# Kernel optimization log

Hardware: AMD Instinct MI355X
Metric: run time of the kernel (lower is better)

Reference implementation:

```python
import jax, jax.numpy as jnp
import numpy as np

BITS = 4
N_PACK = 32 // BITS  # 8
GROUPSIZE = 128
IN_FEATURES = 4096
OUT_FEATURES = 4096


def setup_inputs() -> dict:
    key = jax.random.key(0)
    k1, k2, k3, k4 = jax.random.split(key, 4)
    x = jax.random.normal(k1, (4, 2048, IN_FEATURES), dtype=jnp.float32)
    packed_weight = jax.random.randint(
        k2, (OUT_FEATURES, IN_FEATURES // N_PACK),
        jnp.iinfo(jnp.int32).min, jnp.iinfo(jnp.int32).max, dtype=jnp.int32)
    scale = jax.random.uniform(k3, (OUT_FEATURES, IN_FEATURES // GROUPSIZE),
                               dtype=jnp.float32, minval=0.001, maxval=0.02)
    bias = jax.random.normal(k4, (OUT_FEATURES,), dtype=jnp.float32) * 0.01
    return {"x": x, "packed_weight": packed_weight, "scale": scale, "bias": bias}


def _dequant_weight(packed_weight, scale):
    # Unpack 8 signed int4 values per int32 word (symmetric path, no zero-point).
    # Matches torch recover(): (w << (32 - bits*(n_pack - e))) >> (32 - bits)
    # with arithmetic right shift giving sign extension into int8 range [-8, 7].
    e = jnp.arange(N_PACK, dtype=jnp.int32)
    left = (32 - BITS * (N_PACK - e)).astype(jnp.int32)          # [n_pack]
    w = jnp.right_shift(
        jnp.left_shift(packed_weight[:, :, None], left[None, None, :]),
        32 - BITS)                                               # [O, P, n_pack]
    w = w.reshape(OUT_FEATURES, IN_FEATURES).astype(jnp.float32)
    # Per-group scale: in_features divisible by groupsize (no-remainder branch).
    w = (w.reshape(-1, GROUPSIZE) * scale.reshape(-1, 1)).reshape(OUT_FEATURES, IN_FEATURES)
    return w


def reference(x, packed_weight, scale, bias):
    w = _dequant_weight(packed_weight, scale)      # [O, I] fp32
    # F.linear: x @ w.T + bias
    return jnp.einsum('bsi,oi->bso', x, w) + bias
```

## Files before the change

### kernel.cpp

```cpp
#include <hip/hip_runtime.h>

typedef __bf16 bf16x4 __attribute__((ext_vector_type(4)));
typedef __bf16 bf16x8 __attribute__((ext_vector_type(8)));
typedef float  f32x4  __attribute__((ext_vector_type(4)));

#define M_DIM 8192
#define N_DIM 4096
#define K_DIM 4096

#define GLDS16(gptr, lptr)                                                     \
  __builtin_amdgcn_global_load_lds(                                            \
      (const __attribute__((address_space(1))) void*)(gptr),                   \
      (__attribute__((address_space(3))) void*)(lptr), 16, 0, 0)


__global__ __launch_bounds__(256) void dequant_w_kernel(
    const int* __restrict__ pw, const float* __restrict__ scale,
    unsigned short* __restrict__ wbf) {
  int idx = blockIdx.x * 256 + threadIdx.x;
  int o = idx >> 9;
  int p = idx & 511;
  int w = pw[idx];
  float s = scale[o * 32 + (p >> 4)];
  bf16x8 v;
#pragma unroll
  for (int e = 0; e < 8; ++e) {
    int val = (int)((unsigned)w << (4 * e)) >> 28;
    v[e] = (__bf16)((float)val * s);
  }
  *(bf16x8*)&wbf[(size_t)idx * 8] = v;
}

__global__ __launch_bounds__(256) void conv_x_kernel(
    const float* __restrict__ x, unsigned short* __restrict__ xbf) {
  size_t i = (size_t)(blockIdx.x * 256 + threadIdx.x) * 4;
  float4 a = *(const float4*)&x[i];
  bf16x4 v = {(__bf16)a.x, (__bf16)a.y, (__bf16)a.z, (__bf16)a.w};
  *(bf16x4*)&xbf[i] = v;
}


template <int QM, int QN>
__device__ __forceinline__ void mfma_quad(f32x4 (&acc)[8][4],
                                          const bf16x8 (&a)[4][2],
                                          const bf16x8 (&b)[2][2]) {
  __builtin_amdgcn_s_setprio(1);
#pragma unroll
  for (int mi = 0; mi < 4; ++mi)
#pragma unroll
    for (int ni = 0; ni < 2; ++ni)
#pragma unroll
      for (int kk = 0; kk < 2; ++kk)
        acc[QM * 4 + mi][QN * 2 + ni] =
            __builtin_amdgcn_mfma_f32_16x16x32_bf16(
                a[mi][kk], b[ni][kk], acc[QM * 4 + mi][QN * 2 + ni], 0, 0, 0);
  __builtin_amdgcn_s_setprio(0);
}

#define STAGE_A(qm_, tau_)                                                     \
  do {                                                                         \
    const int k0_ = ((tau_) & 63) * 64;                                        \
    char* const base_ = lds + ((tau_) & 1) * 32768;                            \
    const int c0_ = wave * 2, c1_ = wave * 2 + 1;                              \
    const int R0_ = (qm_) * 64 + (c0_ & 7) * 8 + (c0_ >> 3) * 128;             \
    const int R1_ = (qm_) * 64 + (c1_ & 7) * 8 + (c1_ >> 3) * 128;             \
    GLDS16(xbf + (size_t)(m0 + R0_ + rs8) * K_DIM + k0_ + cs8e,                \
           base_ + R0_ * 128);                                                 \
    GLDS16(xbf + (size_t)(m0 + R1_ + rs8) * K_DIM + k0_ + cs8e,                \
           base_ + R1_ * 128);                                                 \
  } while (0)

#define STAGE_B(qn_, tau_)                                                     \
  do {                                                                         \
    const int k0_ = ((tau_) & 63) * 64;                                        \
    char* const base_ = lds + 65536 + ((tau_) & 1) * 32768;                    \
    const int c0_ = wave * 2, c1_ = wave * 2 + 1;                              \
    const int R0_ = (qn_) * 32 + (c0_ >> 2) * 64 + (c0_ & 3) * 8;              \
    const int R1_ = (qn_) * 32 + (c1_ >> 2) * 64 + (c1_ & 3) * 8;              \
    GLDS16(wbf + (size_t)(n0 + R0_ + rs8) * K_DIM + k0_ + cs8e,                \
           base_ + R0_ * 128);                                                 \
    GLDS16(wbf + (size_t)(n0 + R1_ + rs8) * K_DIM + k0_ + cs8e,                \
           base_ + R1_ * 128);                                                 \
  } while (0)

#define READ_A(d_, qm_)                                                        \
  do {                                                                         \
    const char* pA_ = lds + (d_) * 32768 + (qm_) * 8192 + aRowOff;             \
    a[0][0] = *(const bf16x8*)(pA_ + 0 + b0);                                  \
    a[0][1] = *(const bf16x8*)(pA_ + 0 + b1);                                  \
    a[1][0] = *(const bf16x8*)(pA_ + 2048 + b0);                               \
    a[1][1] = *(const bf16x8*)(pA_ + 2048 + b1);                               \
    a[2][0] = *(const bf16x8*)(pA_ + 4096 + b0);                               \
    a[2][1] = *(const bf16x8*)(pA_ + 4096 + b1);                               \
    a[3][0] = *(const bf16x8*)(pA_ + 6144 + b0);                               \
    a[3][1] = *(const bf16x8*)(pA_ + 6144 + b1);                               \
  } while (0)

#define READ_B(d_, qn_, dst_)                                                  \
  do {                                                                         \
    const char* pB_ = lds + 65536 + (d_) * 32768 + (qn_) * 4096 + bRowOff;     \
    dst_[0][0] = *(const bf16x8*)(pB_ + 0 + b0);                               \
    dst_[0][1] = *(const bf16x8*)(pB_ + 0 + b1);                               \
    dst_[1][0] = *(const bf16x8*)(pB_ + 2048 + b0);                            \
    dst_[1][1] = *(const bf16x8*)(pB_ + 2048 + b1);                            \
  } while (0)

#define PH_MID                                                                 \
  do {                                                                         \
    asm volatile("" ::: "memory");                                             \
    __builtin_amdgcn_s_barrier();                                              \
  } while (0)

#define PH_END                                                                 \
  do {                                                                         \
    asm volatile("" ::: "memory");                                             \
    __builtin_amdgcn_s_barrier();                                              \
  } while (0)

#define VMW6 asm volatile("s_waitcnt vmcnt(6)" ::: "memory")

__global__ __launch_bounds__(512, 2) void gemm8_kernel(
    const unsigned short* __restrict__ xbf,
    const unsigned short* __restrict__ wbf,
    const float* __restrict__ bias, float* __restrict__ out) {
  __shared__ char lds[131072];

  int bid = blockIdx.x;
  int cpx = gridDim.x >> 3;
  int swz = (bid & 7) * cpx + (bid >> 3);
  int bm = swz >> 4;
  int bn = swz & 15;
  int m0 = bm * 256, n0 = bn * 256;

  int tid = threadIdx.x;
  int lane = tid & 63;
  int wave = tid >> 6;
  int wm = wave >> 2, wn = wave & 3;
  int lr = lane & 15, lk = lane >> 4, l7 = lane & 7;

  const int rs8 = lane >> 3;
  const int cs8e = ((lane & 7) ^ rs8) * 8;
  const int b0 = ((lk ^ l7) << 4);
  const int b1 = b0 ^ 64;
  const int aRowOff = (wm * 128 + lr) * 128;
  const int bRowOff = (wn * 64 + lr) * 128;

  f32x4 acc[8][4];
#pragma unroll
  for (int i = 0; i < 8; ++i)
#pragma unroll
    for (int jx = 0; jx < 4; ++jx) acc[i][jx] = (f32x4)0.0f;

  bf16x8 a[4][2], bq0[2][2], bq1[2][2];

  STAGE_A(0, 0);
  STAGE_B(1, 0);
  STAGE_A(1, 0);
  STAGE_B(0, 0);
  STAGE_A(0, 1);
  STAGE_B(1, 1);
  STAGE_A(1, 1);
  VMW6;
  asm volatile("" ::: "memory");
  __builtin_amdgcn_s_barrier();

  for (int j = 0; j < K_DIM / 128; ++j) {
    int t = 2 * j;
    READ_B(0, 0, bq0);
    READ_A(0, 0);
    STAGE_B(0, t + 1);
    PH_MID;
    mfma_quad<0, 0>(acc, a, bq0);
    PH_END;
    READ_B(0, 1, bq1);
    STAGE_A(0, t + 2);
    PH_MID;
    mfma_quad<0, 1>(acc, a, bq1);
    PH_END;
    READ_A(0, 1);
    STAGE_B(1, t + 2);
    PH_MID;
    mfma_quad<1, 1>(acc, a, bq1);
    PH_END;
    STAGE_A(1, t + 2);
    VMW6;
    PH_MID;
    mfma_quad<1, 0>(acc, a, bq0);
    PH_END;
    READ_B(1, 0, bq0);
    READ_A(1, 0);
    STAGE_B(0, t + 2);
    PH_MID;
    mfma_quad<0, 0>(acc, a, bq0);
    PH_END;
    READ_B(1, 1, bq1);
    STAGE_A(0, t + 3);
    PH_MID;
    mfma_quad<0, 1>(acc, a, bq1);
    PH_END;
    READ_A(1, 1);
    STAGE_B(1, t + 3);
    PH_MID;
    mfma_quad<1, 1>(acc, a, bq1);
    PH_END;
    STAGE_A(1, t + 3);
    VMW6;
    PH_MID;
    mfma_quad<1, 0>(acc, a, bq0);
    PH_END;
  }

  asm volatile("s_waitcnt vmcnt(0)" ::: "memory");

#pragma unroll
  for (int ng = 0; ng < 4; ++ng) {
    int col = n0 + wn * 64 + ng * 16 + lr;
    float bv = bias[col];
#pragma unroll
    for (int mg = 0; mg < 8; ++mg) {
      size_t rowb = (size_t)m0 + wm * 128 + mg * 16 + lk * 4;
#pragma unroll
      for (int r = 0; r < 4; ++r)
        out[(rowb + r) * N_DIM + col] = acc[mg][ng][r] + bv;
    }
  }
}

__global__ __launch_bounds__(256) void gemm_fused_kernel(
    const float* __restrict__ x, const int* __restrict__ pw,
    const float* __restrict__ scale, const float* __restrict__ bias,
    float* __restrict__ out) {
  __shared__ unsigned short As[128 * 64];
  __shared__ unsigned short Bs[128 * 64];
  int bid = blockIdx.x;
  int cpx = gridDim.x >> 3;
  int swz = (bid & 7) * cpx + (bid >> 3);
  int bm = swz >> 5, bn = swz & 31;
  int m0 = bm * 128, n0 = bn * 128;
  int tid = threadIdx.x;
  int lane = tid & 63;
  int wave = tid >> 6;
  int wm = wave >> 1, wn = wave & 1;
  int lr = lane & 15, lk = lane >> 4;
  f32x4 acc[4][4];
#pragma unroll
  for (int i = 0; i < 4; ++i)
#pragma unroll
    for (int jx = 0; jx < 4; ++jx) acc[i][jx] = (f32x4)0.0f;
  int tr = tid >> 4, tc = tid & 15;
  float4 ra[8];
  int4 rb;
  float sB = 0.f;
#pragma unroll
  for (int i = 0; i < 8; ++i)
    ra[i] = *(const float4*)&x[(size_t)(m0 + i * 16 + tr) * K_DIM + tc * 4];
  rb = *(const int4*)&pw[(size_t)(n0 + (tid >> 1)) * 512 + (tid & 1) * 4];
  sB = scale[(size_t)(n0 + (tid >> 1)) * 32 + 0];
  const int NT = K_DIM / 64;
  for (int t = 0; t < NT; ++t) {
#pragma unroll
    for (int i = 0; i < 8; ++i) {
      float4 v = ra[i];
      bf16x4 b4 = {(__bf16)v.x, (__bf16)v.y, (__bf16)v.z, (__bf16)v.w};
      *(bf16x4*)&As[(i * 16 + tr) * 64 + tc * 4] = b4;
    }
    {
      int n = tid >> 1, h = tid & 1;
#pragma unroll
      for (int w = 0; w < 4; ++w) {
        int word = ((const int*)&rb)[w];
        bf16x8 o;
#pragma unroll
        for (int e = 0; e < 8; ++e) {
          int val = (int)((unsigned)word << (4 * e)) >> 28;
          o[e] = (__bf16)((float)val * sB);
        }
        *(bf16x8*)&Bs[n * 64 + h * 32 + w * 8] = o;
      }
    }
    if (t + 1 < NT) {
      int k1 = (t + 1) * 64;
#pragma unroll
      for (int i = 0; i < 8; ++i)
        ra[i] = *(const float4*)&x[(size_t)(m0 + i * 16 + tr) * K_DIM + k1 +
                                   tc * 4];
      rb = *(const int4*)&pw[(size_t)(n0 + (tid >> 1)) * 512 + (k1 >> 3) +
                             (tid & 1) * 4];
      sB = scale[(size_t)(n0 + (tid >> 1)) * 32 + (k1 >> 7)];
    }
    __syncthreads();
#pragma unroll
    for (int kk = 0; kk < 2; ++kk) {
      bf16x8 af[4], bfr[4];
#pragma unroll
      for (int mi = 0; mi < 4; ++mi)
        af[mi] = *(const bf16x8*)&As[(wm * 64 + mi * 16 + lr) * 64 + kk * 32 +
                                     lk * 8];
#pragma unroll
      for (int ni = 0; ni < 4; ++ni)
        bfr[ni] = *(const bf16x8*)&Bs[(wn * 64 + ni * 16 + lr) * 64 + kk * 32 +
                                      lk * 8];
#pragma unroll
      for (int mi = 0; mi < 4; ++mi)
#pragma unroll
        for (int ni = 0; ni < 4; ++ni)
          acc[mi][ni] = __builtin_amdgcn_mfma_f32_16x16x32_bf16(
              af[mi], bfr[ni], acc[mi][ni], 0, 0, 0);
    }
    __syncthreads();
  }
#pragma unroll
  for (int ni = 0; ni < 4; ++ni) {
    int col = n0 + wn * 64 + ni * 16 + lr;
    float bv = bias[col];
#pragma unroll
    for (int mi = 0; mi < 4; ++mi) {
      int rowb = m0 + wm * 64 + mi * 16 + lk * 4;
#pragma unroll
      for (int r = 0; r < 4; ++r)
        out[(size_t)(rowb + r) * N_DIM + col] = acc[mi][ni][r] + bv;
    }
  }
}

extern "C" void kernel_launch(void* const* d_in, const int* in_sizes, int n_in,
                              void* d_out, int out_size, void* d_ws,
                              size_t ws_size, hipStream_t stream) {
  const float* x = (const float*)d_in[0];
  const int* pw = (const int*)d_in[1];
  const float* scale = (const float*)d_in[2];
  const float* bias = (const float*)d_in[3];
  float* out = (float*)d_out;

  const size_t needB = (size_t)N_DIM * K_DIM * 2;
  const size_t needA = (size_t)M_DIM * K_DIM * 2;

  if (ws_size >= needA + needB) {
    unsigned short* wbf = (unsigned short*)d_ws;
    unsigned short* xbf = (unsigned short*)((char*)d_ws + needB);
    dequant_w_kernel<<<(N_DIM * (K_DIM / 8)) / 256, 256, 0, stream>>>(pw, scale,
                                                                      wbf);
    conv_x_kernel<<<((size_t)M_DIM * K_DIM / 4) / 256, 256, 0, stream>>>(x,
                                                                         xbf);
    gemm8_kernel<<<(M_DIM / 256) * (N_DIM / 256), 512, 0, stream>>>(xbf, wbf,
                                                                    bias, out);
  } else {
    gemm_fused_kernel<<<(M_DIM / 128) * (N_DIM / 128), 256, 0, stream>>>(
        x, pw, scale, bias, out);
  }
}
```

Measured before the change: 451.0 us.

## Double-buffer A fragments in registers and reorder MFMA quadrant schedule

```diff
diff --git a/kernel.cpp b/kernel.cpp
--- a/kernel.cpp
+++ b/kernel.cpp
@@ -83,17 +83,17 @@
            base_ + R1_ * 128);                                                 \
   } while (0)
 
-#define READ_A(d_, qm_)                                                        \
+#define READ_A2(d_, qm_, dst_)                                                 \
   do {                                                                         \
     const char* pA_ = lds + (d_) * 32768 + (qm_) * 8192 + aRowOff;             \
-    a[0][0] = *(const bf16x8*)(pA_ + 0 + b0);                                  \
-    a[0][1] = *(const bf16x8*)(pA_ + 0 + b1);                                  \
-    a[1][0] = *(const bf16x8*)(pA_ + 2048 + b0);                               \
-    a[1][1] = *(const bf16x8*)(pA_ + 2048 + b1);                               \
-    a[2][0] = *(const bf16x8*)(pA_ + 4096 + b0);                               \
-    a[2][1] = *(const bf16x8*)(pA_ + 4096 + b1);                               \
-    a[3][0] = *(const bf16x8*)(pA_ + 6144 + b0);                               \
-    a[3][1] = *(const bf16x8*)(pA_ + 6144 + b1);                               \
+    dst_[0][0] = *(const bf16x8*)(pA_ + 0 + b0);                               \
+    dst_[0][1] = *(const bf16x8*)(pA_ + 0 + b1);                               \
+    dst_[1][0] = *(const bf16x8*)(pA_ + 2048 + b0);                            \
+    dst_[1][1] = *(const bf16x8*)(pA_ + 2048 + b1);                            \
+    dst_[2][0] = *(const bf16x8*)(pA_ + 4096 + b0);                            \
+    dst_[2][1] = *(const bf16x8*)(pA_ + 4096 + b1);                            \
+    dst_[3][0] = *(const bf16x8*)(pA_ + 6144 + b0);                            \
+    dst_[3][1] = *(const bf16x8*)(pA_ + 6144 + b1);                            \
   } while (0)
 
 #define READ_B(d_, qn_, dst_)                                                  \
@@ -151,62 +151,65 @@
 #pragma unroll
     for (int jx = 0; jx < 4; ++jx) acc[i][jx] = (f32x4)0.0f;
 
-  bf16x8 a[4][2], bq0[2][2], bq1[2][2];
-
+  bf16x8 aQ0[4][2], aQ1[4][2], bQ0[2][2], bQ1[2][2];
+
+  STAGE_B(0, 0);
   STAGE_A(0, 0);
   STAGE_B(1, 0);
   STAGE_A(1, 0);
-  STAGE_B(0, 0);
+  STAGE_B(0, 1);
   STAGE_A(0, 1);
   STAGE_B(1, 1);
   STAGE_A(1, 1);
-  VMW6;
+  asm volatile("s_waitcnt vmcnt(8)" ::: "memory");
   asm volatile("" ::: "memory");
   __builtin_amdgcn_s_barrier();
+  READ_B(0, 0, bQ0);
+  READ_A2(0, 0, aQ0);
 
   for (int j = 0; j < K_DIM / 128; ++j) {
     int t = 2 * j;
-    READ_B(0, 0, bq0);
-    READ_A(0, 0);
-    STAGE_B(0, t + 1);
-    PH_MID;
-    mfma_quad<0, 0>(acc, a, bq0);
-    PH_END;
-    READ_B(0, 1, bq1);
+    READ_B(0, 1, bQ1);
+    STAGE_B(0, t + 2);
+    PH_MID;
+    mfma_quad<0, 0>(acc, aQ0, bQ0);
+    PH_END;
+    READ_A2(0, 1, aQ1);
     STAGE_A(0, t + 2);
     PH_MID;
-    mfma_quad<0, 1>(acc, a, bq1);
-    PH_END;
-    READ_A(0, 1);
+    mfma_quad<0, 1>(acc, aQ0, bQ1);
+    PH_END;
     STAGE_B(1, t + 2);
-    PH_MID;
-    mfma_quad<1, 1>(acc, a, bq1);
-    PH_END;
+    VMW6;
+    PH_MID;
+    mfma_quad<1, 0>(acc, aQ1, bQ0);
+    PH_END;
+    READ_B(1, 0, bQ0);
+    READ_A2(1, 0, aQ0);
     STAGE_A(1, t + 2);
+    PH_MID;
+    mfma_quad<1, 1>(acc, aQ1, bQ1);
+    PH_END;
+    READ_B(1, 1, bQ1);
+    STAGE_B(0, t + 3);
+    PH_MID;
+    mfma_quad<0, 0>(acc, aQ0, bQ0);
+    PH_END;
+    READ_A2(1, 1, aQ1);
+    STAGE_A(0, t + 3);
+    PH_MID;
+    mfma_quad<0, 1>(acc, aQ0, bQ1);
+    PH_END;
+    STAGE_B(1, t + 3);
     VMW6;
     PH_MID;
-    mfma_quad<1, 0>(acc, a, bq0);
-    PH_END;
-    READ_B(1, 0, bq0);
-    READ_A(1, 0);
-    STAGE_B(0, t + 2);
-    PH_MID;
-    mfma_quad<0, 0>(acc, a, bq0);
-    PH_END;
-    READ_B(1, 1, bq1);
-    STAGE_A(0, t + 3);
-    PH_MID;
-    mfma_quad<0, 1>(acc, a, bq1);
-    PH_END;
-    READ_A(1, 1);
-    STAGE_B(1, t + 3);
-    PH_MID;
-    mfma_quad<1, 1>(acc, a, bq1);
-    PH_END;
+    mfma_quad<1, 0>(acc, aQ1, bQ0);
+    PH_END;
+    READ_B(0, 0, bQ0);
+    READ_A2(0, 0, aQ0);
     STAGE_A(1, t + 3);
-    VMW6;
-    PH_MID;
-    mfma_quad<1, 0>(acc, a, bq0);
+    PH_MID;
+    mfma_quad<1, 1>(acc, aQ1, bQ1);
     PH_END;
   }
 
```

Result: slower. 609.9 us (+35.2%).
